# Performance work log

Measured on AMD Instinct MI355X. Metric: run time of the kernel, lower is better.

## Reference

```python
import jax, jax.numpy as jnp
import numpy as np

B, S, D, H = 4, 2048, 1024, 16
DK = D // H


def setup_inputs() -> dict:
    key = jax.random.key(0)
    ks = jax.random.split(key, 10)
    s = 0.02  # keep linear outputs well-scaled
    causal = jnp.triu(jnp.ones((S, S), dtype=bool), k=1)  # True = masked
    return {
        "Q": jax.random.normal(ks[0], (B, S, D), dtype=jnp.float32),
        "K_V": jax.random.normal(ks[1], (B, S, D), dtype=jnp.float32),
        "mask": jnp.broadcast_to(causal, (B, S, S)),
        "Wq": jax.random.normal(ks[2], (D, D), dtype=jnp.float32) * s,
        "bq": jnp.zeros((D,), dtype=jnp.float32),
        "Wk": jax.random.normal(ks[3], (D, D), dtype=jnp.float32) * s,
        "bk": jnp.zeros((D,), dtype=jnp.float32),
        "Wv": jax.random.normal(ks[4], (D, D), dtype=jnp.float32) * s,
        "bv": jnp.zeros((D,), dtype=jnp.float32),
        "Wo": jax.random.normal(ks[5], (D, D), dtype=jnp.float32) * s,
        "bo": jnp.zeros((D,), dtype=jnp.float32),
    }


def reference(Q, K_V, mask, Wq, bq, Wk, bk, Wv, bv, Wo, bo):
    # Linear projections
    q = Q @ Wq + bq          # [B, Sq, D]
    k = K_V @ Wk + bk        # [B, Sk, D]
    v = K_V @ Wv + bv        # [B, Sk, D]
    Sq, Sk = q.shape[1], k.shape[1]
    # chunk(dim=2)+cat(dim=0) == split into H heads of size DK
    q = q.reshape(B, Sq, H, DK)
    k = k.reshape(B, Sk, H, DK)
    v = v.reshape(B, Sk, H, DK)
    scale = 1.0 / jnp.sqrt(jnp.float32(DK))
    scores = jnp.einsum("bqhd,bkhd->bhqk", q, k) * scale  # [B,H,Sq,Sk]
    # mask.repeat(head_num,1,1) == broadcast mask over heads
    scores = jnp.where(mask[:, None, :, :], -jnp.inf, scores)
    attn = jax.nn.softmax(scores, axis=-1)
    # dropout is identity in eval mode
    out = jnp.einsum("bhqk,bkhd->bqhd", attn, v).reshape(B, Sq, D)
    return out @ Wo + bo
```

## Files before the change

kernel.cpp:

```cpp
#include <hip/hip_runtime.h>

typedef unsigned short u16;
typedef __attribute__((ext_vector_type(8))) __bf16 bf16x8;
typedef __attribute__((ext_vector_type(4))) float f32x4;

#define B_  4
#define S_  2048
#define D_  1024
#define H_  16
#define DK_ 64

__device__ __forceinline__ u16 f2bf(float f) {
  unsigned u = __float_as_uint(f);
  u += 0x7fffu + ((u >> 16) & 1u);
  return (u16)(u >> 16);
}
__device__ __forceinline__ u16 f2bf_trunc(float f) {
  return (u16)(__float_as_uint(f) >> 16);
}
__device__ __forceinline__ float hexp2(float f) {
  return __builtin_amdgcn_exp2f(f);
}

__device__ __forceinline__ void load_lds16(const u16* g, u16* l) {
  __builtin_amdgcn_global_load_lds((const __attribute__((address_space(1))) void*)g,
                                   (__attribute__((address_space(3))) void*)l,
                                   16, 0, 0);
}

__global__ void cvt_bf16_2(const float* __restrict__ x0, u16* __restrict__ y0,
                           const float* __restrict__ x1, u16* __restrict__ y1, int n4) {
  int i = blockIdx.x * blockDim.x + threadIdx.x;
  const float* x = x0; u16* y = y0;
  int j = i;
  if (i >= n4) { x = x1; y = y1; j = i - n4; }
  float4 v = ((const float4*)x)[j];
  ushort4 o;
  o.x = f2bf(v.x); o.y = f2bf(v.y); o.z = f2bf(v.z); o.w = f2bf(v.w);
  ((ushort4*)y)[j] = o;
}

__global__ void transpose_cvt4(const float* __restrict__ W0, const float* __restrict__ W1,
                               const float* __restrict__ W2, const float* __restrict__ W3,
                               u16* __restrict__ T0, u16* __restrict__ T1,
                               u16* __restrict__ T2, u16* __restrict__ T3) {
  __shared__ float tile[32][33];
  const float* W = (blockIdx.z == 0) ? W0 : (blockIdx.z == 1) ? W1 : (blockIdx.z == 2) ? W2 : W3;
  u16*         T = (blockIdx.z == 0) ? T0 : (blockIdx.z == 1) ? T1 : (blockIdx.z == 2) ? T2 : T3;
  int bx = blockIdx.x * 32, by = blockIdx.y * 32;
  int tx = threadIdx.x, ty = threadIdx.y;
  #pragma unroll
  for (int i = 0; i < 32; i += 8)
    tile[ty + i][tx] = W[(size_t)(by + ty + i) * D_ + bx + tx];
  __syncthreads();
  #pragma unroll
  for (int i = 0; i < 32; i += 8)
    T[(size_t)(bx + ty + i) * D_ + by + tx] = f2bf(tile[tx][ty + i]);
}

#define GBM 128
#define GBN 256
#define GNT 16

template<int MODE>
__global__ __launch_bounds__(512, 2)
void gemm8p(const u16* __restrict__ Aq, const u16* __restrict__ Ak,
            const u16* __restrict__ Bt,
            const float* __restrict__ bq, const float* __restrict__ bk,
            const float* __restrict__ bv,
            u16* __restrict__ qp, u16* __restrict__ kp, u16* __restrict__ vpT,
            float* __restrict__ Cf, float qscale) {
  __shared__ __align__(16) u16 sm[2 * 24576];
  const int tid  = threadIdx.x;
  const int lane = tid & 63, wave = tid >> 6;
  const int bm = blockIdx.x * GBM;
  const int bn = blockIdx.y * GBN;
  const int wm = (wave >> 2) * 64, wn = (wave & 3) * 64;
  const int fm = lane & 15, fk4 = lane >> 4;
  const int K = D_;

  int path = 0;
  const u16* A = Aq;
  if constexpr (MODE == 0) { path = bn >> 10; if (path != 0) A = Ak; }

  const int sr  = tid >> 2;
  const int sl  = tid & 3;
  const int kof = (sl ^ (sr & 3)) * 8;
  const u16* gA  = A  + (size_t)(bm + sr) * K + kof;
  const u16* gB0 = Bt + (size_t)(bn + sr) * K + kof;
  const u16* gB1 = Bt + (size_t)(bn + 128 + sr) * K + kof;

#define GR(t, ks) do { \
    u16* lr_ = &sm[((t) & 1) * 24576 + (ks) * 12288]; \
    const int ko_ = (t) * 64 + (ks) * 32; \
    load_lds16(gA  + ko_, lr_ + tid * 8); \
    load_lds16(gB0 + ko_, lr_ + 4096 + tid * 8); \
    load_lds16(gB1 + ko_, lr_ + 8192 + tid * 8); \
  } while (0)

  const int sfrag = (fk4 ^ (fm & 3)) * 8;
  f32x4 acc[4][4] = {};

  GR(0, 0);
  asm volatile("" ::: "memory");
  GR(0, 1);
  asm volatile("" ::: "memory");
  GR(1, 0);

  #pragma unroll
  for (int t = 0; t < GNT; ++t) {
    #pragma unroll
    for (int ks = 0; ks < 2; ++ks) {
      if (t < GNT - 1)  asm volatile("s_waitcnt vmcnt(6)" ::: "memory");
      else if (ks == 0) asm volatile("s_waitcnt vmcnt(3)" ::: "memory");
      else              asm volatile("s_waitcnt vmcnt(0)" ::: "memory");
      __builtin_amdgcn_s_barrier();
      if (ks == 0) { if (t + 1 < GNT) GR(t + 1, 1); }
      else         { if (t + 2 < GNT) GR(t + 2, 0); }
      asm volatile("" ::: "memory");

      const u16* rb = &sm[(t & 1) * 24576 + ks * 12288];
      bf16x8 af[4], bfr[4];
      #pragma unroll
      for (int m = 0; m < 4; ++m)
        af[m] = *(const bf16x8*)&rb[(wm + m * 16 + fm) * 32 + sfrag];
      #pragma unroll
      for (int j = 0; j < 4; ++j)
        bfr[j] = *(const bf16x8*)&rb[(128 + wn + j * 16 + fm) * 32 + sfrag];
      asm volatile("s_waitcnt lgkmcnt(0)" ::: "memory");
      __builtin_amdgcn_s_setprio(1);
      #pragma unroll
      for (int m = 0; m < 4; ++m)
        #pragma unroll
        for (int j = 0; j < 4; ++j)
          acc[m][j] = __builtin_amdgcn_mfma_f32_16x16x32_bf16(af[m], bfr[j], acc[m][j], 0, 0, 0);
      __builtin_amdgcn_s_setprio(0);
    }
  }
#undef GR

  if constexpr (MODE == 0) {
    #pragma unroll
    for (int i = 0; i < 4; ++i) {
      #pragma unroll
      for (int j = 0; j < 4; ++j) {
        int colg = bn + wn + j * 16 + fm;
        int rowg0 = bm + wm + i * 16 + fk4 * 4;
        if (path == 0) {
          float bb = bq[colg];
          #pragma unroll
          for (int rg = 0; rg < 4; ++rg)
            qp[(size_t)(rowg0 + rg) * D_ + colg] = f2bf((acc[i][j][rg] + bb) * qscale);
        } else if (path == 1) {
          int ck = colg - 1024;
          float bb = bk[ck];
          #pragma unroll
          for (int rg = 0; rg < 4; ++rg)
            kp[(size_t)(rowg0 + rg) * D_ + ck] = f2bf(acc[i][j][rg] + bb);
        } else {
          int cv = colg - 2048;
          float bb = bv[cv];
          int hh = cv >> 6, dk = cv & 63;
          int bbt = rowg0 >> 11, s = rowg0 & (S_ - 1);
          ushort4 pk4;
          pk4.x = f2bf(acc[i][j][0] + bb);
          pk4.y = f2bf(acc[i][j][1] + bb);
          pk4.z = f2bf(acc[i][j][2] + bb);
          pk4.w = f2bf(acc[i][j][3] + bb);
          *(ushort4*)&vpT[(((size_t)bbt * H_ + hh) * DK_ + dk) * S_ + s] = pk4;
        }
      }
    }
  } else {
    #pragma unroll
    for (int i = 0; i < 4; ++i)
      #pragma unroll
      for (int j = 0; j < 4; ++j) {
        int colg = bn + wn + j * 16 + fm;
        float bb = bq[colg];
        #pragma unroll
        for (int rg = 0; rg < 4; ++rg) {
          int rowg = bm + wm + i * 16 + fk4 * 4 + rg;
          Cf[(size_t)rowg * D_ + colg] = acc[i][j][rg] + bb;
        }
      }
  }
}

#define PST 136

__global__ __launch_bounds__(256, 2)
void attn_kernel(const u16* __restrict__ qp, const u16* __restrict__ kp,
                 const u16* __restrict__ vpT, u16* __restrict__ ao) {
  __shared__ u16 Ks[16 * 512];
  __shared__ u16 Vs[16 * 512];
  __shared__ u16 Ps[4 * 32 * PST];

  const int tid  = threadIdx.x;
  const int lane = tid & 63;
  const int w    = tid >> 6;
  const int fm   = lane & 15;
  const int fk4  = lane >> 4;

  const int i = blockIdx.x;
  const int b = i & 3;
  const int h = (i >> 2) & 15;
  const int p = i >> 6;

  u16* Pw = &Ps[w * 32 * PST];
  const u16* kb = kp  + (size_t)(b * S_) * D_ + h * DK_;
  const u16* vb = vpT + (size_t)((b * H_ + h) * DK_) * S_;

  #pragma unroll 1
  for (int sidx = 0; sidx < 2; ++sidx) {
    const int qt = (sidx == 0) ? p : 15 - p;
    const int q0 = qt * 128 + w * 32;
    const int nj = qt + 1;

    bf16x8 aq[2][2];
    #pragma unroll
    for (int qf = 0; qf < 2; ++qf)
      #pragma unroll
      for (int kh = 0; kh < 2; ++kh)
        aq[qf][kh] = *(const bf16x8*)(qp + (size_t)(b * S_ + q0 + qf * 16 + fm) * D_
                                         + h * DK_ + kh * 32 + fk4 * 8);

    f32x4 oacc[2][4] = {};
    float l0 = 0.f, l1 = 0.f;

    #pragma unroll 1
    for (int j = 0; j < nj; ++j) {
      const int kv0 = j * 128;
      const bool lastt = (j == qt);

      __syncthreads();
      #pragma unroll
      for (int c = 0; c < 4; ++c) {
        int idx = 4 * w + c;
        load_lds16(kb + (size_t)(kv0 + (idx >> 1) * 16 + fm) * D_ + (idx & 1) * 32 + fk4 * 8,
                   &Ks[idx * 512 + lane * 8]);
      }
      #pragma unroll
      for (int c = 0; c < 4; ++c) {
        int idx = 4 * w + c;
        load_lds16(vb + (size_t)((idx & 3) * 16 + fm) * S_ + kv0 + (idx >> 2) * 32 + fk4 * 8,
                   &Vs[idx * 512 + lane * 8]);
      }
      __syncthreads();

      #pragma unroll
      for (int mt = 0; mt < 8; ++mt) {
        bf16x8 kf0 = *(const bf16x8*)&Ks[(mt * 2 + 0) * 512 + lane * 8];
        bf16x8 kf1 = *(const bf16x8*)&Ks[(mt * 2 + 1) * 512 + lane * 8];
        f32x4 z0 = {0.f, 0.f, 0.f, 0.f}, z1 = z0;
        z0 = __builtin_amdgcn_mfma_f32_16x16x32_bf16(kf0, aq[0][0], z0, 0, 0, 0);
        z0 = __builtin_amdgcn_mfma_f32_16x16x32_bf16(kf1, aq[0][1], z0, 0, 0, 0);
        z1 = __builtin_amdgcn_mfma_f32_16x16x32_bf16(kf0, aq[1][0], z1, 0, 0, 0);
        z1 = __builtin_amdgcn_mfma_f32_16x16x32_bf16(kf1, aq[1][1], z1, 0, 0, 0);

        const int kvr = kv0 + mt * 16 + fk4 * 4;
        ushort4 p0, p1;
        #pragma unroll
        for (int rg = 0; rg < 4; ++rg) {
          float zz0 = z0[rg], zz1 = z1[rg];
          if (lastt) {
            if (kvr + rg > q0 + fm)      zz0 = -1e30f;
            if (kvr + rg > q0 + 16 + fm) zz1 = -1e30f;
          }
          float e0 = hexp2(zz0);
          float e1 = hexp2(zz1);
          l0 += e0; l1 += e1;
          ((u16*)&p0)[rg] = f2bf_trunc(e0);
          ((u16*)&p1)[rg] = f2bf_trunc(e1);
        }
        *(ushort4*)&Pw[(fm)      * PST + mt * 16 + fk4 * 4] = p0;
        *(ushort4*)&Pw[(16 + fm) * PST + mt * 16 + fk4 * 4] = p1;
      }

      #pragma unroll
      for (int kt = 0; kt < 4; ++kt) {
        bf16x8 ap0 = *(const bf16x8*)&Pw[(fm)      * PST + kt * 32 + fk4 * 8];
        bf16x8 ap1 = *(const bf16x8*)&Pw[(16 + fm) * PST + kt * 32 + fk4 * 8];
        #pragma unroll
        for (int nt = 0; nt < 4; ++nt) {
          bf16x8 bv = *(const bf16x8*)&Vs[(kt * 4 + nt) * 512 + lane * 8];
          oacc[0][nt] = __builtin_amdgcn_mfma_f32_16x16x32_bf16(ap0, bv, oacc[0][nt], 0, 0, 0);
          oacc[1][nt] = __builtin_amdgcn_mfma_f32_16x16x32_bf16(ap1, bv, oacc[1][nt], 0, 0, 0);
        }
      }
    }

    #pragma unroll
    for (int qf = 0; qf < 2; ++qf) {
      float ls = (qf == 0) ? l0 : l1;
      ls += __shfl_xor(ls, 16, 64);
      ls += __shfl_xor(ls, 32, 64);
      #pragma unroll
      for (int rg = 0; rg < 4; ++rg) {
        float lr = __shfl(ls, fk4 * 4 + rg, 64);
        float inv = 1.0f / lr;
        int q = q0 + qf * 16 + fk4 * 4 + rg;
        #pragma unroll
        for (int nt = 0; nt < 4; ++nt) {
          float o = oacc[qf][nt][rg] * inv;
          ao[(size_t)(b * S_ + q) * D_ + h * DK_ + nt * 16 + fm] = f2bf(o);
        }
      }
    }
  }
}

extern "C" void kernel_launch(void* const* d_in, const int* in_sizes, int n_in,
                              void* d_out, int out_size, void* d_ws, size_t ws_size,
                              hipStream_t stream) {
  const float* Q  = (const float*)d_in[0];
  const float* KV = (const float*)d_in[1];
  const float* Wq = (const float*)d_in[3];
  const float* bq = (const float*)d_in[4];
  const float* Wk = (const float*)d_in[5];
  const float* bk = (const float*)d_in[6];
  const float* Wv = (const float*)d_in[7];
  const float* bv = (const float*)d_in[8];
  const float* Wo = (const float*)d_in[9];
  const float* bo = (const float*)d_in[10];
  float* out = (float*)d_out;

  char* ws = (char*)d_ws;
  u16* Qb  = (u16*)(ws);
  u16* Kb  = (u16*)(ws + (16ull << 20));
  u16* Wqt = (u16*)(ws + (32ull << 20));
  u16* Wkt = (u16*)(ws + (34ull << 20));
  u16* Wvt = (u16*)(ws + (36ull << 20));
  u16* Wot = (u16*)(ws + (38ull << 20));
  u16* qp  = (u16*)(ws + (40ull << 20));
  u16* kp  = (u16*)(ws + (56ull << 20));
  u16* vpT = (u16*)(ws + (72ull << 20));
  u16* ao  = Qb;

  const int n4 = (B_ * S_ * D_) / 4;
  cvt_bf16_2<<<2 * n4 / 256, 256, 0, stream>>>(Q, Qb, KV, Kb, n4);

  transpose_cvt4<<<dim3(32, 32, 4), dim3(32, 8), 0, stream>>>(Wq, Wk, Wv, Wo,
                                                              Wqt, Wkt, Wvt, Wot);

  const float qscale = 0.125f * 1.44269504f;
  gemm8p<0><<<dim3(8192 / GBM, 3072 / GBN), 512, 0, stream>>>(
      Qb, Kb, Wqt, bq, bk, bv, qp, kp, vpT, nullptr, qscale);

  attn_kernel<<<512, 256, 0, stream>>>(qp, kp, vpT, ao);

  gemm8p<1><<<dim3(8192 / GBM, 1024 / GBN), 512, 0, stream>>>(
      ao, nullptr, Wot, bo, nullptr, nullptr, nullptr, nullptr, nullptr, out, 1.0f);
}
```

Before: 329.9 us.

## Split attention into one q-tile per block, shrink P buffer, raise occupancy

The attention kernel now launches 1024 blocks, each handling one 128-row query tile, scheduled heaviest first, instead of 512 blocks that each process a paired light and heavy tile. The P staging buffer is halved by processing the key tile in two 64-wide halves and writing P directly in the MFMA operand fragment layout, with perm-based bf16 packing. Together with launch bounds raised to 3 blocks per CU, this aims for higher occupancy and better load balance. The cost is that K/V tiles are reloaded more often across blocks, and the causal work per block is uneven, so balance depends on heavy-first ordering.

Result: no change. 332.3 us (+0.8%).

```diff
diff --git a/kernel.cpp b/kernel.cpp
--- a/kernel.cpp
+++ b/kernel.cpp
@@ -15,11 +15,11 @@
   u += 0x7fffu + ((u >> 16) & 1u);
   return (u16)(u >> 16);
 }
-__device__ __forceinline__ u16 f2bf_trunc(float f) {
-  return (u16)(__float_as_uint(f) >> 16);
-}
 __device__ __forceinline__ float hexp2(float f) {
   return __builtin_amdgcn_exp2f(f);
+}
+__device__ __forceinline__ unsigned pack_bf2(float f0, float f1) {
+  return __builtin_amdgcn_perm(__float_as_uint(f1), __float_as_uint(f0), 0x07060302u);
 }
 
 __device__ __forceinline__ void load_lds16(const u16* g, u16* l) {
@@ -187,14 +187,12 @@
   }
 }
 
-#define PST 136
-
-__global__ __launch_bounds__(256, 2)
+__global__ __launch_bounds__(256, 3)
 void attn_kernel(const u16* __restrict__ qp, const u16* __restrict__ kp,
                  const u16* __restrict__ vpT, u16* __restrict__ ao) {
   __shared__ u16 Ks[16 * 512];
   __shared__ u16 Vs[16 * 512];
-  __shared__ u16 Ps[4 * 32 * PST];
+  __shared__ u16 Ps[4 * 4 * 512];
 
   const int tid  = threadIdx.x;
   const int lane = tid & 63;
@@ -202,54 +200,55 @@
   const int fm   = lane & 15;
   const int fk4  = lane >> 4;
 
-  const int i = blockIdx.x;
-  const int b = i & 3;
-  const int h = (i >> 2) & 15;
-  const int p = i >> 6;
-
-  u16* Pw = &Ps[w * 32 * PST];
+  const int i  = blockIdx.x;
+  const int qt = 15 - (i >> 6);
+  const int bh = i & 63;
+  const int b  = bh >> 4;
+  const int h  = bh & 15;
+
+  const int q0 = qt * 128 + w * 32;
+  const int nj = qt + 1;
+
+  u16* Pw = &Ps[w * 2048];
   const u16* kb = kp  + (size_t)(b * S_) * D_ + h * DK_;
   const u16* vb = vpT + (size_t)((b * H_ + h) * DK_) * S_;
 
+  bf16x8 aq[2][2];
+  #pragma unroll
+  for (int qf = 0; qf < 2; ++qf)
+    #pragma unroll
+    for (int kh = 0; kh < 2; ++kh)
+      aq[qf][kh] = *(const bf16x8*)(qp + (size_t)(b * S_ + q0 + qf * 16 + fm) * D_
+                                       + h * DK_ + kh * 32 + fk4 * 8);
+
+  f32x4 oacc[2][4] = {};
+  float l0 = 0.f, l1 = 0.f;
+
   #pragma unroll 1
-  for (int sidx = 0; sidx < 2; ++sidx) {
-    const int qt = (sidx == 0) ? p : 15 - p;
-    const int q0 = qt * 128 + w * 32;
-    const int nj = qt + 1;
-
-    bf16x8 aq[2][2];
-    #pragma unroll
-    for (int qf = 0; qf < 2; ++qf)
-      #pragma unroll
-      for (int kh = 0; kh < 2; ++kh)
-        aq[qf][kh] = *(const bf16x8*)(qp + (size_t)(b * S_ + q0 + qf * 16 + fm) * D_
-                                         + h * DK_ + kh * 32 + fk4 * 8);
-
-    f32x4 oacc[2][4] = {};
-    float l0 = 0.f, l1 = 0.f;
-
-    #pragma unroll 1
-    for (int j = 0; j < nj; ++j) {
-      const int kv0 = j * 128;
-      const bool lastt = (j == qt);
-
-      __syncthreads();
-      #pragma unroll
-      for (int c = 0; c < 4; ++c) {
-        int idx = 4 * w + c;
-        load_lds16(kb + (size_t)(kv0 + (idx >> 1) * 16 + fm) * D_ + (idx & 1) * 32 + fk4 * 8,
-                   &Ks[idx * 512 + lane * 8]);
-      }
-      #pragma unroll
-      for (int c = 0; c < 4; ++c) {
-        int idx = 4 * w + c;
-        load_lds16(vb + (size_t)((idx & 3) * 16 + fm) * S_ + kv0 + (idx >> 2) * 32 + fk4 * 8,
-                   &Vs[idx * 512 + lane * 8]);
-      }
-      __syncthreads();
-
-      #pragma unroll
-      for (int mt = 0; mt < 8; ++mt) {
+  for (int j = 0; j < nj; ++j) {
+    const int kv0 = j * 128;
+    const bool lastt = (j == qt);
+
+    __syncthreads();
+    #pragma unroll
+    for (int c = 0; c < 4; ++c) {
+      int idx = 4 * w + c;
+      load_lds16(kb + (size_t)(kv0 + (idx >> 1) * 16 + fm) * D_ + (idx & 1) * 32 + fk4 * 8,
+                 &Ks[idx * 512 + lane * 8]);
+    }
+    #pragma unroll
+    for (int c = 0; c < 4; ++c) {
+      int idx = 4 * w + c;
+      load_lds16(vb + (size_t)((idx & 3) * 16 + fm) * S_ + kv0 + (idx >> 2) * 32 + fk4 * 8,
+                 &Vs[idx * 512 + lane * 8]);
+    }
+    __syncthreads();
+
+    #pragma unroll
+    for (int h2 = 0; h2 < 2; ++h2) {
+      #pragma unroll
+      for (int mtl = 0; mtl < 4; ++mtl) {
+        const int mt = h2 * 4 + mtl;
         bf16x8 kf0 = *(const bf16x8*)&Ks[(mt * 2 + 0) * 512 + lane * 8];
         bf16x8 kf1 = *(const bf16x8*)&Ks[(mt * 2 + 1) * 512 + lane * 8];
         f32x4 z0 = {0.f, 0.f, 0.f, 0.f}, z1 = z0;
@@ -259,7 +258,7 @@
         z1 = __builtin_amdgcn_mfma_f32_16x16x32_bf16(kf1, aq[1][1], z1, 0, 0, 0);
 
         const int kvr = kv0 + mt * 16 + fk4 * 4;
-        ushort4 p0, p1;
+        float e0[4], e1[4];
         #pragma unroll
         for (int rg = 0; rg < 4; ++rg) {
           float zz0 = z0[rg], zz1 = z1[rg];
@@ -267,20 +266,25 @@
             if (kvr + rg > q0 + fm)      zz0 = -1e30f;
             if (kvr + rg > q0 + 16 + fm) zz1 = -1e30f;
           }
-          float e0 = hexp2(zz0);
-          float e1 = hexp2(zz1);
-          l0 += e0; l1 += e1;
-          ((u16*)&p0)[rg] = f2bf_trunc(e0);
-          ((u16*)&p1)[rg] = f2bf_trunc(e1);
+          e0[rg] = hexp2(zz0);
+          e1[rg] = hexp2(zz1);
+          l0 += e0[rg]; l1 += e1[rg];
         }
-        *(ushort4*)&Pw[(fm)      * PST + mt * 16 + fk4 * 4] = p0;
-        *(ushort4*)&Pw[(16 + fm) * PST + mt * 16 + fk4 * 4] = p1;
-      }
-
-      #pragma unroll
-      for (int kt = 0; kt < 4; ++kt) {
-        bf16x8 ap0 = *(const bf16x8*)&Pw[(fm)      * PST + kt * 32 + fk4 * 8];
-        bf16x8 ap1 = *(const bf16x8*)&Pw[(16 + fm) * PST + kt * 32 + fk4 * 8];
+        const int ktl  = mtl >> 1;
+        const int fk4c = (mt & 1) * 2 + (fk4 >> 1);
+        const int woff = ((fk4c * 16 + fm) * 8 + (fk4 & 1) * 4);
+        uint2 w0, w1;
+        w0.x = pack_bf2(e0[0], e0[1]); w0.y = pack_bf2(e0[2], e0[3]);
+        w1.x = pack_bf2(e1[0], e1[1]); w1.y = pack_bf2(e1[2], e1[3]);
+        *(uint2*)&Pw[(ktl * 2 + 0) * 512 + woff] = w0;
+        *(uint2*)&Pw[(ktl * 2 + 1) * 512 + woff] = w1;
+      }
+
+      #pragma unroll
+      for (int ktl = 0; ktl < 2; ++ktl) {
+        const int kt = h2 * 2 + ktl;
+        bf16x8 ap0 = *(const bf16x8*)&Pw[(ktl * 2 + 0) * 512 + lane * 8];
+        bf16x8 ap1 = *(const bf16x8*)&Pw[(ktl * 2 + 1) * 512 + lane * 8];
         #pragma unroll
         for (int nt = 0; nt < 4; ++nt) {
           bf16x8 bv = *(const bf16x8*)&Vs[(kt * 4 + nt) * 512 + lane * 8];
@@ -289,22 +293,22 @@
         }
       }
     }
-
-    #pragma unroll
-    for (int qf = 0; qf < 2; ++qf) {
-      float ls = (qf == 0) ? l0 : l1;
-      ls += __shfl_xor(ls, 16, 64);
-      ls += __shfl_xor(ls, 32, 64);
-      #pragma unroll
-      for (int rg = 0; rg < 4; ++rg) {
-        float lr = __shfl(ls, fk4 * 4 + rg, 64);
-        float inv = 1.0f / lr;
-        int q = q0 + qf * 16 + fk4 * 4 + rg;
-        #pragma unroll
-        for (int nt = 0; nt < 4; ++nt) {
-          float o = oacc[qf][nt][rg] * inv;
-          ao[(size_t)(b * S_ + q) * D_ + h * DK_ + nt * 16 + fm] = f2bf(o);
-        }
+  }
+
+  #pragma unroll
+  for (int qf = 0; qf < 2; ++qf) {
+    float ls = (qf == 0) ? l0 : l1;
+    ls += __shfl_xor(ls, 16, 64);
+    ls += __shfl_xor(ls, 32, 64);
+    #pragma unroll
+    for (int rg = 0; rg < 4; ++rg) {
+      float lr = __shfl(ls, fk4 * 4 + rg, 64);
+      float inv = 1.0f / lr;
+      int q = q0 + qf * 16 + fk4 * 4 + rg;
+      #pragma unroll
+      for (int nt = 0; nt < 4; ++nt) {
+        float o = oacc[qf][nt][rg] * inv;
+        ao[(size_t)(b * S_ + q) * D_ + h * DK_ + nt * 16 + fm] = f2bf(o);
       }
     }
   }
@@ -347,7 +351,7 @@
   gemm8p<0><<<dim3(8192 / GBM, 3072 / GBN), 512, 0, stream>>>(
       Qb, Kb, Wqt, bq, bk, bv, qp, kp, vpT, nullptr, qscale);
 
-  attn_kernel<<<512, 256, 0, stream>>>(qp, kp, vpT, ao);
+  attn_kernel<<<1024, 256, 0, stream>>>(qp, kp, vpT, ao);
 
   gemm8p<1><<<dim3(8192 / GBM, 1024 / GBN), 512, 0, stream>>>(
       ao, nullptr, Wot, bo, nullptr, nullptr, nullptr, nullptr, nullptr, out, 1.0f);
```
